# Performance work log

Measured on AMD Instinct MI355X. Metric: run time of the kernel, lower is better.

Reference implementation:

```python
import jax, jax.numpy as jnp
import numpy as np

HEAD_SIZE = 64
NEG_INF = float('-inf')


def setup_inputs() -> dict:
    key = jax.random.key(0)
    ks = jax.random.split(key, 4)
    B, S, H, D = 8, 4096, 1024, HEAD_SIZE
    scale = 1.0 / np.sqrt(H)
    return {
        'x': jax.random.normal(ks[0], (B, S, H), dtype=jnp.float32),
        'Wq': jax.random.normal(ks[1], (H, D), dtype=jnp.float32) * scale,
        'bq': jnp.zeros((D,), dtype=jnp.float32),
        'Wk': jax.random.normal(ks[2], (H, D), dtype=jnp.float32) * scale,
        'bk': jnp.zeros((D,), dtype=jnp.float32),
        'Wv': jax.random.normal(ks[3], (H, D), dtype=jnp.float32) * scale,
        'bv': jnp.zeros((D,), dtype=jnp.float32),
    }


def reference(x, Wq, bq, Wk, bk, Wv, bv):
    # x: [B, S, H]; projections -> [B, S, D]
    B, S, H = x.shape
    q = jnp.einsum('bsh,hd->bsd', x, Wq) + bq
    k = jnp.einsum('bsh,hd->bsd', x, Wk) + bk
    v = jnp.einsum('bsh,hd->bsd', x, Wv) + bv
    # raw scores [B, S, S]
    scores = jnp.einsum('bqd,bkd->bqk', q, k)
    # causal mask applied BEFORE scaling (matches original; -inf/scale == -inf)
    causal = jnp.tril(jnp.ones((S, S), dtype=bool))
    scores = jnp.where(causal, scores, NEG_INF)
    scale = 1.0 / jnp.sqrt(jnp.asarray(q.shape[-1], dtype=scores.dtype))
    attn = jax.nn.softmax(scores * scale, axis=-1)
    # dropout = 0.0 (eval) -> identity
    return jnp.einsum('bqk,bkd->bqd', attn, v)
```

## Files before the change

kernel.cpp:

```cpp
#include <hip/hip_runtime.h>
#include <hip/hip_bf16.h>
#include <math.h>

#define SEQ 4096
#define HID 1024
#define DH  64
#define NB  8
#define QSCALE 0.18033688011112042f

typedef unsigned short ushort_t;
typedef unsigned int   uint_t;
typedef __attribute__((ext_vector_type(8))) short  bf16x8;
typedef __attribute__((ext_vector_type(4))) float  f32x4;
typedef __attribute__((ext_vector_type(4))) uint_t u32x4;
typedef __attribute__((ext_vector_type(2))) uint_t u32x2;

static __device__ __forceinline__ ushort_t f2bf(float f) {
    __hip_bfloat16 h = __float2bfloat16(f);
    return *reinterpret_cast<ushort_t*>(&h);
}
static __device__ __forceinline__ ushort_t f2bf_fast(float f) {
    uint_t u = __float_as_uint(f);
    return (ushort_t)((u + 0x8000u) >> 16);
}
static __device__ __forceinline__ uint_t bfpair(float lo, float hi) {
    return (uint_t)f2bf_fast(lo) | ((uint_t)f2bf_fast(hi) << 16);
}

static __device__ __forceinline__ void gld_lds16(const void* g, void* s) {
    __builtin_amdgcn_global_load_lds(
        (const __attribute__((address_space(1))) void*)g,
        (__attribute__((address_space(3))) void*)s, 16, 0, 0);
}

__global__ __launch_bounds__(256) void prep_w(
    const float* __restrict__ Wq, const float* __restrict__ Wk,
    const float* __restrict__ Wv, ushort_t* __restrict__ wts)
{
    __shared__ ushort_t tr[64][72];
    const int bx   = blockIdx.x;
    const int mmat = bx >> 4;
    const int kt   = bx & 15;
    const float* W  = (mmat == 0) ? Wq : (mmat == 1) ? Wk : Wv;
    const float  sc = (mmat == 0) ? QSCALE : 1.0f;

    const int t  = threadIdx.x;
    const int kr = t >> 2, kc = (t & 3) * 16;
    const float* src = W + (size_t)(kt * 64 + kr) * DH + kc;
    float4 a0 = *(const float4*)(src);
    float4 a1 = *(const float4*)(src + 4);
    float4 a2 = *(const float4*)(src + 8);
    float4 a3 = *(const float4*)(src + 12);
    float vv[16] = {a0.x,a0.y,a0.z,a0.w, a1.x,a1.y,a1.z,a1.w,
                    a2.x,a2.y,a2.z,a2.w, a3.x,a3.y,a3.z,a3.w};
    #pragma unroll
    for (int i = 0; i < 16; ++i) tr[kr][kc + i] = f2bf(vv[i] * sc);
    __syncthreads();

    const int cl = t >> 2, jc = (t & 3) * 16;
    const int c  = mmat * 64 + cl;
    ushort_t* dst = wts + kt * 12288 + c * 64;
    #pragma unroll
    for (int jj = 0; jj < 16; ++jj) {
        int j = jc + jj;
        dst[((j >> 3) ^ (cl & 7)) * 8 + (j & 7)] = tr[j][cl];
    }
}

__global__ __launch_bounds__(256) void qkv_proj(
    const float* __restrict__ x, const ushort_t* __restrict__ wts,
    const float* __restrict__ bq, const float* __restrict__ bk,
    const float* __restrict__ bv,
    ushort_t* __restrict__ qimg, ushort_t* __restrict__ kimg,
    ushort_t* __restrict__ vimg)
{
    __shared__ ushort_t bw[2][12288];

    const int t  = threadIdx.x;
    const int w  = t >> 6, l = t & 63, lr = l & 15, g = l >> 4;
    const int row0 = blockIdx.x * 64;
    const int row  = row0 + w * 16 + lr;
    const int ch0 = (g ^ (lr & 7)) * 8;
    const int ch1 = ((g + 4) ^ (lr & 7)) * 8;

    f32x4 acc[12];
    #pragma unroll
    for (int i = 0; i < 12; ++i) acc[i] = (f32x4){0.f,0.f,0.f,0.f};

    const char* wbase = (const char*)wts;
    const int   wlo   = w * 1024 + l * 16;
    const float* xrow = x + (size_t)row * HID + g * 8;

    float4 Xa0, Xa1, Xb0, Xb1;
    {
        Xa0 = *(const float4*)(xrow);
        Xa1 = *(const float4*)(xrow + 4);
        Xb0 = *(const float4*)(xrow + 32);
        Xb1 = *(const float4*)(xrow + 36);
        char* bdst = (char*)&bw[0][0] + w * 1024;
        #pragma unroll
        for (int i = 0; i < 6; ++i)
            gld_lds16(wbase + wlo + i * 4096, bdst + i * 4096);
    }

    for (int kt = 0; kt < 16; ++kt) {
        const int buf = kt & 1;
        __syncthreads();
        float4 Na0, Na1, Nb0, Nb1;
        if (kt < 15) {
            const float* xn = xrow + (kt + 1) * 64;
            Na0 = *(const float4*)(xn);
            Na1 = *(const float4*)(xn + 4);
            Nb0 = *(const float4*)(xn + 32);
            Nb1 = *(const float4*)(xn + 36);
            char* bdst = (char*)&bw[buf ^ 1][0] + w * 1024;
            const char* bsrc = wbase + (size_t)(kt + 1) * 24576 + wlo;
            #pragma unroll
            for (int i = 0; i < 6; ++i)
                gld_lds16(bsrc + i * 4096, bdst + i * 4096);
        }
        bf16x8 af0, af1;
        {
            u32x4 p;
            p.x = bfpair(Xa0.x, Xa0.y); p.y = bfpair(Xa0.z, Xa0.w);
            p.z = bfpair(Xa1.x, Xa1.y); p.w = bfpair(Xa1.z, Xa1.w);
            af0 = *(bf16x8*)&p;
            u32x4 q;
            q.x = bfpair(Xb0.x, Xb0.y); q.y = bfpair(Xb0.z, Xb0.w);
            q.z = bfpair(Xb1.x, Xb1.y); q.w = bfpair(Xb1.z, Xb1.w);
            af1 = *(bf16x8*)&q;
        }
        #pragma unroll
        for (int ct = 0; ct < 12; ++ct) {
            const int c = ct * 16 + lr;
            bf16x8 b0 = *(bf16x8*)&bw[buf][c * 64 + ch0];
            bf16x8 b1 = *(bf16x8*)&bw[buf][c * 64 + ch1];
            acc[ct] = __builtin_amdgcn_mfma_f32_16x16x32_bf16(af0, b0, acc[ct], 0, 0, 0);
            acc[ct] = __builtin_amdgcn_mfma_f32_16x16x32_bf16(af1, b1, acc[ct], 0, 0, 0);
        }
        Xa0 = Na0; Xa1 = Na1; Xb0 = Nb0; Xb1 = Nb1;
    }

    #pragma unroll
    for (int ct = 0; ct < 12; ++ct) {
        const int c    = ct * 16 + lr;
        const int mmat = c >> 6;
        const int cc   = c & 63;
        const float* bp = (mmat == 0) ? bq : (mmat == 1) ? bk : bv;
        const float bias = bp[cc] * (mmat == 0 ? QSCALE : 1.0f);
        #pragma unroll
        for (int r = 0; r < 4; ++r) {
            const int s = row0 + w * 16 + g * 4 + r;
            const ushort_t v = f2bf_fast(acc[ct][r] + bias);
            if (mmat == 0)
                qimg[(size_t)s * 64 + cc] = v;
            else if (mmat == 1)
                kimg[(size_t)(s >> 6) * 4096 + (s & 63) * 64 +
                     ((cc >> 3) ^ (s & 7)) * 8 + (cc & 7)] = v;
            else
                vimg[(size_t)(s >> 6) * 4096 + (size_t)cc * 64 +
                     (((s & 63) >> 3) ^ (cc & 7)) * 8 + (s & 7)] = v;
        }
    }
}

__global__ __launch_bounds__(256) void attn(
    const ushort_t* __restrict__ qimg, const ushort_t* __restrict__ kimg,
    const ushort_t* __restrict__ vimg,
    float* __restrict__ Opart, float* __restrict__ Lpart)
{
    __shared__ ushort_t kvs[2][8192];
    __shared__ ushort_t ps[64][72];

    const int t  = threadIdx.x;
    const int w  = t >> 6, l = t & 63, lr = l & 15, g = l >> 4;
    const int bx   = blockIdx.x;
    const int half = bx & 1;
    const int u    = bx >> 1;
    const int qt   = 63 - (u >> 3);
    const int b    = u & 7;
    const int q0   = qt * 64;
    const int n    = qt + 1, h = n >> 1;
    const int t0   = half ? h : 0;
    const int t1   = half ? n : h;
    const int ch0 = (g ^ (lr & 7)) * 8;
    const int ch1 = ((g + 4) ^ (lr & 7)) * 8;
    const int qq  = q0 + w * 16 + lr;

    bf16x8 qf0, qf1;
    {
        const ushort_t* qp = qimg + (size_t)(b * SEQ + qq) * 64 + g * 8;
        qf0 = *(const bf16x8*)(qp);
        qf1 = *(const bf16x8*)(qp + 32);
    }

    f32x4 o[4];
    #pragma unroll
    for (int dt = 0; dt < 4; ++dt) o[dt] = (f32x4){0.f,0.f,0.f,0.f};
    float lpart = 0.f;

    const char* kbase = (const char*)kimg + (size_t)b * 524288;
    const char* vbase = (const char*)vimg + (size_t)b * 524288;
    const int wo = w * 1024;
    const int lo = l * 16;

    if (t0 < t1) {
        const char* ks = kbase + (size_t)t0 * 8192;
        const char* vs = vbase + (size_t)t0 * 8192;
        char* lk = (char*)&kvs[0][0];
        gld_lds16(ks + wo + lo,        lk + wo);
        gld_lds16(ks + wo + lo + 4096, lk + wo + 4096);
        gld_lds16(vs + wo + lo,        lk + wo + 8192);
        gld_lds16(vs + wo + lo + 4096, lk + wo + 12288);
    }

    for (int kt = t0; kt < t1; ++kt) {
        const int cur = (kt - t0) & 1;
        __syncthreads();
        if (kt + 1 < t1) {
            const char* ks = kbase + (size_t)(kt + 1) * 8192;
            const char* vs = vbase + (size_t)(kt + 1) * 8192;
            char*       lk = (char*)&kvs[cur ^ 1][0];
            gld_lds16(ks + wo + lo,        lk + wo);
            gld_lds16(ks + wo + lo + 4096, lk + wo + 4096);
            gld_lds16(vs + wo + lo,        lk + wo + 8192);
            gld_lds16(vs + wo + lo + 4096, lk + wo + 12288);
        }

        const ushort_t* kb = &kvs[cur][0];
        f32x4 s[4];
        #pragma unroll
        for (int ct = 0; ct < 4; ++ct) {
            const int rowb = (ct * 16 + lr) * 64;
            bf16x8 kf0 = *(const bf16x8*)(kb + rowb + ch0);
            bf16x8 kf1 = *(const bf16x8*)(kb + rowb + ch1);
            s[ct] = (f32x4){0.f,0.f,0.f,0.f};
            s[ct] = __builtin_amdgcn_mfma_f32_16x16x32_bf16(kf0, qf0, s[ct], 0, 0, 0);
            s[ct] = __builtin_amdgcn_mfma_f32_16x16x32_bf16(kf1, qf1, s[ct], 0, 0, 0);
        }

        if (kt == qt) {
            const int kvb = kt * 64 + g * 4;
            #pragma unroll
            for (int ct = 0; ct < 4; ++ct) {
                float p0 = ((kvb + ct*16 + 0) > qq) ? 0.f : __builtin_amdgcn_exp2f(s[ct][0]);
                float p1 = ((kvb + ct*16 + 1) > qq) ? 0.f : __builtin_amdgcn_exp2f(s[ct][1]);
                float p2 = ((kvb + ct*16 + 2) > qq) ? 0.f : __builtin_amdgcn_exp2f(s[ct][2]);
                float p3 = ((kvb + ct*16 + 3) > qq) ? 0.f : __builtin_amdgcn_exp2f(s[ct][3]);
                lpart += (p0 + p1) + (p2 + p3);
                u32x2 pk = { bfpair(p0, p1), bfpair(p2, p3) };
                *(u32x2*)&ps[w * 16 + lr][ct * 16 + g * 4] = pk;
            }
        } else {
            #pragma unroll
            for (int ct = 0; ct < 4; ++ct) {
                float p0 = __builtin_amdgcn_exp2f(s[ct][0]);
                float p1 = __builtin_amdgcn_exp2f(s[ct][1]);
                float p2 = __builtin_amdgcn_exp2f(s[ct][2]);
                float p3 = __builtin_amdgcn_exp2f(s[ct][3]);
                lpart += (p0 + p1) + (p2 + p3);
                u32x2 pk = { bfpair(p0, p1), bfpair(p2, p3) };
                *(u32x2*)&ps[w * 16 + lr][ct * 16 + g * 4] = pk;
            }
        }
        asm volatile("s_waitcnt lgkmcnt(0)" ::: "memory");

        bf16x8 pf0 = *(const bf16x8*)&ps[w * 16 + lr][g * 8];
        bf16x8 pf1 = *(const bf16x8*)&ps[w * 16 + lr][32 + g * 8];
        const ushort_t* vb = &kvs[cur][4096];
        #pragma unroll
        for (int dt = 0; dt < 4; ++dt) {
            const int rowb = (dt * 16 + lr) * 64;
            bf16x8 vf0 = *(const bf16x8*)(vb + rowb + ch0);
            bf16x8 vf1 = *(const bf16x8*)(vb + rowb + ch1);
            o[dt] = __builtin_amdgcn_mfma_f32_16x16x32_bf16(vf0, pf0, o[dt], 0, 0, 0);
            o[dt] = __builtin_amdgcn_mfma_f32_16x16x32_bf16(vf1, pf1, o[dt], 0, 0, 0);
        }
    }

    lpart += __shfl_xor(lpart, 16);
    lpart += __shfl_xor(lpart, 32);

    const int m = b * 64 + qt;
    float* Op = Opart + ((size_t)half * 512 + m) * 4096;
    #pragma unroll
    for (int dt = 0; dt < 4; ++dt)
        *(f32x4*)&Op[(w * 16 + lr) * 64 + dt * 16 + g * 4] = o[dt];
    if (g == 0)
        Lpart[((size_t)half * 512 + m) * 64 + w * 16 + lr] = lpart;
}

__global__ __launch_bounds__(256) void merge_o(
    const float* __restrict__ Opart, const float* __restrict__ Lpart,
    float* __restrict__ outg)
{
    const int m = blockIdx.x;
    const int b = m >> 6, qt = m & 63;
    const int t = threadIdx.x;
    const int row = t >> 2, c = (t & 3) * 16;

    const float* A = Opart + (size_t)m * 4096 + row * 64 + c;
    const float* B = Opart + (size_t)(512 + m) * 4096 + row * 64 + c;
    const float la = Lpart[(size_t)m * 64 + row];
    const float lb = Lpart[(size_t)(512 + m) * 64 + row];
    const float inv = 1.0f / (la + lb);
    float* dst = outg + ((size_t)b * SEQ + qt * 64 + row) * 64 + c;
    #pragma unroll
    for (int j = 0; j < 4; ++j) {
        float4 va = *(const float4*)(A + j * 4);
        float4 vb = *(const float4*)(B + j * 4);
        float4 vo = { (va.x + vb.x) * inv, (va.y + vb.y) * inv,
                      (va.z + vb.z) * inv, (va.w + vb.w) * inv };
        *(float4*)(dst + j * 4) = vo;
    }
}

extern "C" void kernel_launch(void* const* d_in, const int* in_sizes, int n_in,
                              void* d_out, int out_size, void* d_ws, size_t ws_size,
                              hipStream_t stream) {
    const float* x  = (const float*)d_in[0];
    const float* Wq = (const float*)d_in[1];
    const float* bq = (const float*)d_in[2];
    const float* Wk = (const float*)d_in[3];
    const float* bk = (const float*)d_in[4];
    const float* Wv = (const float*)d_in[5];
    const float* bv = (const float*)d_in[6];
    float* out = (float*)d_out;

    const size_t per = (size_t)NB * SEQ * DH;
    ushort_t* q   = (ushort_t*)d_ws;
    ushort_t* k   = q + per;
    ushort_t* v   = k + per;
    ushort_t* wts = v + per;
    float* Opart  = (float*)((char*)d_ws + (size_t)(16u << 20));
    float* Lpart  = (float*)((char*)d_ws + (size_t)(40u << 20));

    prep_w  <<<dim3(48),   256, 0, stream>>>(Wq, Wk, Wv, wts);
    qkv_proj<<<dim3(512),  256, 0, stream>>>(x, wts, bq, bk, bv, q, k, v);
    attn    <<<dim3(1024), 256, 0, stream>>>(q, k, v, Opart, Lpart);
    merge_o <<<dim3(512),  256, 0, stream>>>(Opart, Lpart, out);
}
```

Before: 261.8 us.

## Drop split-KV attention and merge kernel; write normalized output directly

Each attention block now handles a full causal query tile instead of half of its KV range, so the partial O/L buffers and the separate merge kernel go away and output is normalized in-register. Query tiles are ordered longest-first for the first half of the grid and shortest-first for the second half to balance load across 512 blocks. s_setprio is raised around the MFMA sections to favor matrix issue. The cost is half as many blocks and longer per-block serial loops, which may lower occupancy and worsen tail imbalance.

```diff
diff --git a/kernel.cpp b/kernel.cpp
--- a/kernel.cpp
+++ b/kernel.cpp
@@ -166,23 +166,19 @@
 
 __global__ __launch_bounds__(256) void attn(
     const ushort_t* __restrict__ qimg, const ushort_t* __restrict__ kimg,
-    const ushort_t* __restrict__ vimg,
-    float* __restrict__ Opart, float* __restrict__ Lpart)
+    const ushort_t* __restrict__ vimg, float* __restrict__ outg)
 {
     __shared__ ushort_t kvs[2][8192];
     __shared__ ushort_t ps[64][72];
 
     const int t  = threadIdx.x;
     const int w  = t >> 6, l = t & 63, lr = l & 15, g = l >> 4;
-    const int bx   = blockIdx.x;
-    const int half = bx & 1;
-    const int u    = bx >> 1;
-    const int qt   = 63 - (u >> 3);
-    const int b    = u & 7;
-    const int q0   = qt * 64;
-    const int n    = qt + 1, h = n >> 1;
-    const int t0   = half ? h : 0;
-    const int t1   = half ? n : h;
+    const int bx = blockIdx.x;
+    const int b  = bx & 7;
+    const int m  = bx >> 3;
+    const int qt = (m < 32) ? (63 - m) : (m - 32);
+    const int q0 = qt * 64;
+    const int nt = qt + 1;
     const int ch0 = (g ^ (lr & 7)) * 8;
     const int ch1 = ((g + 4) ^ (lr & 7)) * 8;
     const int qq  = q0 + w * 16 + lr;
@@ -204,20 +200,18 @@
     const int wo = w * 1024;
     const int lo = l * 16;
 
-    if (t0 < t1) {
-        const char* ks = kbase + (size_t)t0 * 8192;
-        const char* vs = vbase + (size_t)t0 * 8192;
+    {
         char* lk = (char*)&kvs[0][0];
-        gld_lds16(ks + wo + lo,        lk + wo);
-        gld_lds16(ks + wo + lo + 4096, lk + wo + 4096);
-        gld_lds16(vs + wo + lo,        lk + wo + 8192);
-        gld_lds16(vs + wo + lo + 4096, lk + wo + 12288);
-    }
-
-    for (int kt = t0; kt < t1; ++kt) {
-        const int cur = (kt - t0) & 1;
+        gld_lds16(kbase + wo + lo,        lk + wo);
+        gld_lds16(kbase + wo + lo + 4096, lk + wo + 4096);
+        gld_lds16(vbase + wo + lo,        lk + wo + 8192);
+        gld_lds16(vbase + wo + lo + 4096, lk + wo + 12288);
+    }
+
+    for (int kt = 0; kt < nt; ++kt) {
+        const int cur = kt & 1;
         __syncthreads();
-        if (kt + 1 < t1) {
+        if (kt + 1 < nt) {
             const char* ks = kbase + (size_t)(kt + 1) * 8192;
             const char* vs = vbase + (size_t)(kt + 1) * 8192;
             char*       lk = (char*)&kvs[cur ^ 1][0];
@@ -229,6 +223,7 @@
 
         const ushort_t* kb = &kvs[cur][0];
         f32x4 s[4];
+        __builtin_amdgcn_s_setprio(1);
         #pragma unroll
         for (int ct = 0; ct < 4; ++ct) {
             const int rowb = (ct * 16 + lr) * 64;
@@ -238,6 +233,7 @@
             s[ct] = __builtin_amdgcn_mfma_f32_16x16x32_bf16(kf0, qf0, s[ct], 0, 0, 0);
             s[ct] = __builtin_amdgcn_mfma_f32_16x16x32_bf16(kf1, qf1, s[ct], 0, 0, 0);
         }
+        __builtin_amdgcn_s_setprio(0);
 
         if (kt == qt) {
             const int kvb = kt * 64 + g * 4;
@@ -268,6 +264,7 @@
         bf16x8 pf0 = *(const bf16x8*)&ps[w * 16 + lr][g * 8];
         bf16x8 pf1 = *(const bf16x8*)&ps[w * 16 + lr][32 + g * 8];
         const ushort_t* vb = &kvs[cur][4096];
+        __builtin_amdgcn_s_setprio(1);
         #pragma unroll
         for (int dt = 0; dt < 4; ++dt) {
             const int rowb = (dt * 16 + lr) * 64;
@@ -276,42 +273,18 @@
             o[dt] = __builtin_amdgcn_mfma_f32_16x16x32_bf16(vf0, pf0, o[dt], 0, 0, 0);
             o[dt] = __builtin_amdgcn_mfma_f32_16x16x32_bf16(vf1, pf1, o[dt], 0, 0, 0);
         }
+        __builtin_amdgcn_s_setprio(0);
     }
 
     lpart += __shfl_xor(lpart, 16);
     lpart += __shfl_xor(lpart, 32);
-
-    const int m = b * 64 + qt;
-    float* Op = Opart + ((size_t)half * 512 + m) * 4096;
-    #pragma unroll
-    for (int dt = 0; dt < 4; ++dt)
-        *(f32x4*)&Op[(w * 16 + lr) * 64 + dt * 16 + g * 4] = o[dt];
-    if (g == 0)
-        Lpart[((size_t)half * 512 + m) * 64 + w * 16 + lr] = lpart;
-}
-
-__global__ __launch_bounds__(256) void merge_o(
-    const float* __restrict__ Opart, const float* __restrict__ Lpart,
-    float* __restrict__ outg)
-{
-    const int m = blockIdx.x;
-    const int b = m >> 6, qt = m & 63;
-    const int t = threadIdx.x;
-    const int row = t >> 2, c = (t & 3) * 16;
-
-    const float* A = Opart + (size_t)m * 4096 + row * 64 + c;
-    const float* B = Opart + (size_t)(512 + m) * 4096 + row * 64 + c;
-    const float la = Lpart[(size_t)m * 64 + row];
-    const float lb = Lpart[(size_t)(512 + m) * 64 + row];
-    const float inv = 1.0f / (la + lb);
-    float* dst = outg + ((size_t)b * SEQ + qt * 64 + row) * 64 + c;
-    #pragma unroll
-    for (int j = 0; j < 4; ++j) {
-        float4 va = *(const float4*)(A + j * 4);
-        float4 vb = *(const float4*)(B + j * 4);
-        float4 vo = { (va.x + vb.x) * inv, (va.y + vb.y) * inv,
-                      (va.z + vb.z) * inv, (va.w + vb.w) * inv };
-        *(float4*)(dst + j * 4) = vo;
+    const float inv = 1.0f / lpart;
+
+    float* dst = outg + ((size_t)b * SEQ + qq) * 64;
+    #pragma unroll
+    for (int dt = 0; dt < 4; ++dt) {
+        f32x4 ov = o[dt] * inv;
+        *(f32x4*)&dst[dt * 16 + g * 4] = ov;
     }
 }
 
@@ -332,11 +305,8 @@
     ushort_t* k   = q + per;
     ushort_t* v   = k + per;
     ushort_t* wts = v + per;
-    float* Opart  = (float*)((char*)d_ws + (size_t)(16u << 20));
-    float* Lpart  = (float*)((char*)d_ws + (size_t)(40u << 20));
-
-    prep_w  <<<dim3(48),   256, 0, stream>>>(Wq, Wk, Wv, wts);
-    qkv_proj<<<dim3(512),  256, 0, stream>>>(x, wts, bq, bk, bv, q, k, v);
-    attn    <<<dim3(1024), 256, 0, stream>>>(q, k, v, Opart, Lpart);
-    merge_o <<<dim3(512),  256, 0, stream>>>(Opart, Lpart, out);
-}
+
+    prep_w  <<<dim3(48),  256, 0, stream>>>(Wq, Wk, Wv, wts);
+    qkv_proj<<<dim3(512), 256, 0, stream>>>(x, wts, bq, bk, bv, q, k, v);
+    attn    <<<dim3(512), 256, 0, stream>>>(q, k, v, out);
+}
```

Result: slower. 277.4 us (+6.0%).

## Switch attention to 32x32x16 MFMA with register P via permlane swap

Applied to the files above, without the earlier changes.

Changes the attention kernel from 16x16x32 MFMA tiles to 32x32x16 tiles. The 2x2 wave grid is split over query halves and key halves. The probability matrix now stays in registers, rearranged with v_permlane32_swap instead of a round trip through LDS with a waitcnt. The two key-half partial outputs are reduced through shared memory at the end. This removes the per-tile LDS store and reload of P and lowers MFMA instruction count. In exchange it adds a final LDS reduction, uses more accumulator registers, and writes the output with scalar-strided global stores.

```diff
diff --git a/kernel.cpp b/kernel.cpp
--- a/kernel.cpp
+++ b/kernel.cpp
@@ -10,10 +10,11 @@
 
 typedef unsigned short ushort_t;
 typedef unsigned int   uint_t;
-typedef __attribute__((ext_vector_type(8))) short  bf16x8;
-typedef __attribute__((ext_vector_type(4))) float  f32x4;
-typedef __attribute__((ext_vector_type(4))) uint_t u32x4;
-typedef __attribute__((ext_vector_type(2))) uint_t u32x2;
+typedef __attribute__((ext_vector_type(8)))  short  bf16x8;
+typedef __attribute__((ext_vector_type(4)))  float  f32x4;
+typedef __attribute__((ext_vector_type(16))) float  f32x16;
+typedef __attribute__((ext_vector_type(4)))  uint_t u32x4;
+typedef __attribute__((ext_vector_type(2)))  uint_t u32x2;
 
 static __device__ __forceinline__ ushort_t f2bf(float f) {
     __hip_bfloat16 h = __float2bfloat16(f);
@@ -170,33 +171,34 @@
     float* __restrict__ Opart, float* __restrict__ Lpart)
 {
     __shared__ ushort_t kvs[2][8192];
-    __shared__ ushort_t ps[64][72];
+    __shared__ float    osc[4096];
+    __shared__ float    lred[2][32];
 
     const int t  = threadIdx.x;
-    const int w  = t >> 6, l = t & 63, lr = l & 15, g = l >> 4;
+    const int w  = t >> 6, l = t & 63, lw = l & 31, hs = l >> 5;
+    const int qh = w & 1;
+    const int kh = w >> 1;
     const int bx   = blockIdx.x;
     const int half = bx & 1;
     const int u    = bx >> 1;
     const int qt   = 63 - (u >> 3);
     const int b    = u & 7;
     const int q0   = qt * 64;
-    const int n    = qt + 1, h = n >> 1;
-    const int t0   = half ? h : 0;
-    const int t1   = half ? n : h;
-    const int ch0 = (g ^ (lr & 7)) * 8;
-    const int ch1 = ((g + 4) ^ (lr & 7)) * 8;
-    const int qq  = q0 + w * 16 + lr;
-
-    bf16x8 qf0, qf1;
+    const int n    = qt + 1, hn = n >> 1;
+    const int t0   = half ? hn : 0;
+    const int t1   = half ? n : hn;
+    const int qq   = q0 + qh * 32 + lw;
+
+    bf16x8 qf[4];
     {
-        const ushort_t* qp = qimg + (size_t)(b * SEQ + qq) * 64 + g * 8;
-        qf0 = *(const bf16x8*)(qp);
-        qf1 = *(const bf16x8*)(qp + 32);
-    }
-
-    f32x4 o[4];
-    #pragma unroll
-    for (int dt = 0; dt < 4; ++dt) o[dt] = (f32x4){0.f,0.f,0.f,0.f};
+        const ushort_t* qp = qimg + (size_t)(b * SEQ + qq) * 64 + hs * 8;
+        #pragma unroll
+        for (int ks = 0; ks < 4; ++ks) qf[ks] = *(const bf16x8*)(qp + ks * 16);
+    }
+
+    f32x16 o0, o1;
+    #pragma unroll
+    for (int r = 0; r < 16; ++r) { o0[r] = 0.f; o1[r] = 0.f; }
     float lpart = 0.f;
 
     const char* kbase = (const char*)kimg + (size_t)b * 524288;
@@ -227,67 +229,101 @@
             gld_lds16(vs + wo + lo + 4096, lk + wo + 12288);
         }
 
-        const ushort_t* kb = &kvs[cur][0];
-        f32x4 s[4];
-        #pragma unroll
-        for (int ct = 0; ct < 4; ++ct) {
-            const int rowb = (ct * 16 + lr) * 64;
-            bf16x8 kf0 = *(const bf16x8*)(kb + rowb + ch0);
-            bf16x8 kf1 = *(const bf16x8*)(kb + rowb + ch1);
-            s[ct] = (f32x4){0.f,0.f,0.f,0.f};
-            s[ct] = __builtin_amdgcn_mfma_f32_16x16x32_bf16(kf0, qf0, s[ct], 0, 0, 0);
-            s[ct] = __builtin_amdgcn_mfma_f32_16x16x32_bf16(kf1, qf1, s[ct], 0, 0, 0);
-        }
-
+        const ushort_t* kb   = &kvs[cur][0];
+        const int       krow = kh * 32 + lw;
+        const ushort_t* krb  = kb + krow * 64;
+        f32x16 s;
+        #pragma unroll
+        for (int r = 0; r < 16; ++r) s[r] = 0.f;
+        #pragma unroll
+        for (int ks = 0; ks < 4; ++ks) {
+            bf16x8 kf = *(const bf16x8*)(krb + (((ks * 2 + hs) ^ (krow & 7)) * 8));
+            s = __builtin_amdgcn_mfma_f32_32x32x16_bf16(kf, qf[ks], s, 0, 0, 0);
+        }
+
+        float p[16];
         if (kt == qt) {
-            const int kvb = kt * 64 + g * 4;
             #pragma unroll
-            for (int ct = 0; ct < 4; ++ct) {
-                float p0 = ((kvb + ct*16 + 0) > qq) ? 0.f : __builtin_amdgcn_exp2f(s[ct][0]);
-                float p1 = ((kvb + ct*16 + 1) > qq) ? 0.f : __builtin_amdgcn_exp2f(s[ct][1]);
-                float p2 = ((kvb + ct*16 + 2) > qq) ? 0.f : __builtin_amdgcn_exp2f(s[ct][2]);
-                float p3 = ((kvb + ct*16 + 3) > qq) ? 0.f : __builtin_amdgcn_exp2f(s[ct][3]);
-                lpart += (p0 + p1) + (p2 + p3);
-                u32x2 pk = { bfpair(p0, p1), bfpair(p2, p3) };
-                *(u32x2*)&ps[w * 16 + lr][ct * 16 + g * 4] = pk;
+            for (int r = 0; r < 16; ++r) {
+                const int kvg = kt * 64 + kh * 32 + (r & 3) + 8 * (r >> 2) + 4 * hs;
+                p[r] = (kvg > qq) ? 0.f : __builtin_amdgcn_exp2f(s[r]);
             }
         } else {
             #pragma unroll
-            for (int ct = 0; ct < 4; ++ct) {
-                float p0 = __builtin_amdgcn_exp2f(s[ct][0]);
-                float p1 = __builtin_amdgcn_exp2f(s[ct][1]);
-                float p2 = __builtin_amdgcn_exp2f(s[ct][2]);
-                float p3 = __builtin_amdgcn_exp2f(s[ct][3]);
-                lpart += (p0 + p1) + (p2 + p3);
-                u32x2 pk = { bfpair(p0, p1), bfpair(p2, p3) };
-                *(u32x2*)&ps[w * 16 + lr][ct * 16 + g * 4] = pk;
+            for (int r = 0; r < 16; ++r) p[r] = __builtin_amdgcn_exp2f(s[r]);
+        }
+        {
+            float s0 = (p[0] + p[1])  + (p[2] + p[3]);
+            float s1 = (p[4] + p[5])  + (p[6] + p[7]);
+            float s2 = (p[8] + p[9])  + (p[10] + p[11]);
+            float s3 = (p[12] + p[13]) + (p[14] + p[15]);
+            lpart += (s0 + s1) + (s2 + s3);
+        }
+
+        const ushort_t* vb = &kvs[cur][4096];
+        #pragma unroll
+        for (int ks2 = 0; ks2 < 2; ++ks2) {
+            uint_t a0 = bfpair(p[ks2*8 + 0], p[ks2*8 + 1]);
+            uint_t b0 = bfpair(p[ks2*8 + 4], p[ks2*8 + 5]);
+            uint_t a1 = bfpair(p[ks2*8 + 2], p[ks2*8 + 3]);
+            uint_t b1 = bfpair(p[ks2*8 + 6], p[ks2*8 + 7]);
+            asm("v_permlane32_swap_b32 %0, %1" : "+v"(a0), "+v"(b0));
+            asm("v_permlane32_swap_b32 %0, %1" : "+v"(a1), "+v"(b1));
+            u32x4 pw = { a0, a1, b0, b1 };
+            bf16x8 paf = *(bf16x8*)&pw;
+            const int sl8 = kh * 4 + ks2 * 2 + hs;
+            {
+                const int vr0 = lw;
+                bf16x8 vf0 = *(const bf16x8*)(vb + vr0 * 64 + ((sl8 ^ (vr0 & 7)) * 8));
+                o0 = __builtin_amdgcn_mfma_f32_32x32x16_bf16(paf, vf0, o0, 0, 0, 0);
+                const int vr1 = 32 + lw;
+                bf16x8 vf1 = *(const bf16x8*)(vb + vr1 * 64 + ((sl8 ^ (vr1 & 7)) * 8));
+                o1 = __builtin_amdgcn_mfma_f32_32x32x16_bf16(paf, vf1, o1, 0, 0, 0);
             }
         }
-        asm volatile("s_waitcnt lgkmcnt(0)" ::: "memory");
-
-        bf16x8 pf0 = *(const bf16x8*)&ps[w * 16 + lr][g * 8];
-        bf16x8 pf1 = *(const bf16x8*)&ps[w * 16 + lr][32 + g * 8];
-        const ushort_t* vb = &kvs[cur][4096];
-        #pragma unroll
-        for (int dt = 0; dt < 4; ++dt) {
-            const int rowb = (dt * 16 + lr) * 64;
-            bf16x8 vf0 = *(const bf16x8*)(vb + rowb + ch0);
-            bf16x8 vf1 = *(const bf16x8*)(vb + rowb + ch1);
-            o[dt] = __builtin_amdgcn_mfma_f32_16x16x32_bf16(vf0, pf0, o[dt], 0, 0, 0);
-            o[dt] = __builtin_amdgcn_mfma_f32_16x16x32_bf16(vf1, pf1, o[dt], 0, 0, 0);
-        }
-    }
-
-    lpart += __shfl_xor(lpart, 16);
-    lpart += __shfl_xor(lpart, 32);
-
-    const int m = b * 64 + qt;
-    float* Op = Opart + ((size_t)half * 512 + m) * 4096;
-    #pragma unroll
-    for (int dt = 0; dt < 4; ++dt)
-        *(f32x4*)&Op[(w * 16 + lr) * 64 + dt * 16 + g * 4] = o[dt];
-    if (g == 0)
-        Lpart[((size_t)half * 512 + m) * 64 + w * 16 + lr] = lpart;
+    }
+
+    if (kh == 1) {
+        const int lbase = (qh * 64 + l) * 32;
+        #pragma unroll
+        for (int i = 0; i < 4; ++i) {
+            f32x4 v = { o0[4*i], o0[4*i+1], o0[4*i+2], o0[4*i+3] };
+            *(f32x4*)&osc[lbase + ((i ^ (l & 7)) * 4)] = v;
+        }
+        #pragma unroll
+        for (int i = 0; i < 4; ++i) {
+            f32x4 v = { o1[4*i], o1[4*i+1], o1[4*i+2], o1[4*i+3] };
+            *(f32x4*)&osc[lbase + (((i + 4) ^ (l & 7)) * 4)] = v;
+        }
+        float lsum = lpart + __shfl_xor(lpart, 32);
+        if (hs == 0) lred[qh][lw] = lsum;
+    }
+    __syncthreads();
+    if (kh == 0) {
+        const int lbase = (qh * 64 + l) * 32;
+        #pragma unroll
+        for (int i = 0; i < 4; ++i) {
+            f32x4 v = *(const f32x4*)&osc[lbase + ((i ^ (l & 7)) * 4)];
+            o0[4*i] += v.x; o0[4*i+1] += v.y; o0[4*i+2] += v.z; o0[4*i+3] += v.w;
+        }
+        #pragma unroll
+        for (int i = 0; i < 4; ++i) {
+            f32x4 v = *(const f32x4*)&osc[lbase + (((i + 4) ^ (l & 7)) * 4)];
+            o1[4*i] += v.x; o1[4*i+1] += v.y; o1[4*i+2] += v.z; o1[4*i+3] += v.w;
+        }
+        const float lt = (lpart + __shfl_xor(lpart, 32)) + lred[qh][lw];
+
+        const int m = b * 64 + qt;
+        float* Op = Opart + ((size_t)half * 512 + m) * 4096;
+        #pragma unroll
+        for (int r = 0; r < 16; ++r) {
+            const int qrow = qh * 32 + (r & 3) + 8 * (r >> 2) + 4 * hs;
+            Op[qrow * 64 + lw]      = o0[r];
+            Op[qrow * 64 + 32 + lw] = o1[r];
+        }
+        if (hs == 0)
+            Lpart[((size_t)half * 512 + m) * 64 + qh * 32 + lw] = lt;
+    }
 }
 
 __global__ __launch_bounds__(256) void merge_o(
```

Measured after the change: 257.1 us. No clear change (-1.8%).
